# Kernel tuning notes

Measured on AMD Instinct MI355X. Metric: run time of the kernel, lower is better.

The kernel has to match this reference:

```python
import jax, jax.numpy as jnp
import numpy as np

MARGIN = 50.0

def setup_inputs() -> dict:
    key = jax.random.key(0)
    k1, k2 = jax.random.split(key)
    N, D = 4096, 768
    rep_anchor = jax.random.normal(k1, (N, D), dtype=jnp.float32)
    rep_pos = jax.random.normal(k2, (N, D), dtype=jnp.float32)
    return {"rep_anchor": rep_anchor, "rep_pos": rep_pos}

def reference(rep_anchor, rep_pos):
    # pairwise euclidean distances: dist[i, j] = ||anchor_i - pos_j||_2
    # (F.pairwise_distance with p=2, eps handled implicitly; use stable sqrt)
    a2 = jnp.sum(rep_anchor * rep_anchor, axis=1, keepdims=True)   # [N,1]
    p2 = jnp.sum(rep_pos * rep_pos, axis=1, keepdims=True).T       # [1,N]
    cross = rep_anchor @ rep_pos.T                                  # [N,N]
    sq = jnp.maximum(a2 + p2 - 2.0 * cross, 0.0)
    dist = jnp.sqrt(sq + 1e-12)
    scores = MARGIN - dist                                          # [N,N]
    # row-wise negative log-softmax, take diagonal (positive pair at index i)
    logp = jax.nn.log_softmax(scores, axis=1)
    loss_per_row = -jnp.diagonal(logp)                               # [N]
    return loss_per_row.mean()
```

## Files before the change

### kernel.cpp

```cpp
#include <hip/hip_runtime.h>
#include <hip/hip_bf16.h>
#include <hip/hip_fp8.h>
#include <stdint.h>


#define N_ROWS 4096
#define D_DIM  768
#define GRID_DIM (N_ROWS / 128)
#define NITER (D_DIM / 64)
#define BUFB  (128 * 64)

typedef float f32x4 __attribute__((ext_vector_type(4)));
typedef int   i32x4 __attribute__((ext_vector_type(4)));

__global__ __launch_bounds__(256) void cvt_norms(
        const float* __restrict__ A, const float* __restrict__ P,
        uint8_t* __restrict__ A8, uint8_t* __restrict__ P8,
        float* __restrict__ a2, float* __restrict__ p2, float* __restrict__ S) {
    const int t = threadIdx.x, lane = t & 63, wave = t >> 6;
    const int row = blockIdx.x * 4 + wave;
    const float* src = blockIdx.y ? P : A;
    uint8_t* dst = blockIdx.y ? P8 : A8;
    float* nrm = blockIdx.y ? p2 : a2;

    const float4* s4 = (const float4*)src + (size_t)row * (D_DIM / 4);
    uint32_t* d4 = (uint32_t*)dst + (size_t)row * (D_DIM / 4);
    float s = 0.0f;
#pragma unroll
    for (int c = 0; c < 3; c++) {
        const int wf = c * 64 + lane;
        float4 v = s4[wf];
        s += v.x * v.x + v.y * v.y + v.z * v.z + v.w * v.w;
        union { uint32_t u; uint8_t b[4]; } pk;
        pk.b[0] = __hip_fp8_e4m3(v.x).__x;
        pk.b[1] = __hip_fp8_e4m3(v.y).__x;
        pk.b[2] = __hip_fp8_e4m3(v.z).__x;
        pk.b[3] = __hip_fp8_e4m3(v.w).__x;
        const int kb = wf >> 4, w16 = wf & 15;
        const int gw = w16 >> 1, h = w16 & 1;
        const int gp = ((gw & 3) << 1) | (gw >> 2);
        d4[(kb << 4) + (gp << 1) + h] = pk.u;
    }
    for (int off = 32; off; off >>= 1) s += __shfl_down(s, off);
    if (lane == 0) {
        nrm[row] = s;
        if (blockIdx.y == 0) S[row] = 0.0f;
    }
}

__device__ __forceinline__ void g2l16(const void* g, void* l) {
    __builtin_amdgcn_global_load_lds(
        (const __attribute__((address_space(1))) void*)g,
        (__attribute__((address_space(3))) void*)l, 16, 0, 0);
}

__global__ __launch_bounds__(256) void gemm_fused(
        const uint8_t* __restrict__ A8, const uint8_t* __restrict__ P8,
        const float* __restrict__ a2, const float* __restrict__ p2,
        float* __restrict__ S, float* __restrict__ Dd) {
    __shared__ __align__(16) uint8_t As[3 * BUFB];
    __shared__ __align__(16) uint8_t Bs[3 * BUFB];

    const int bm = blockIdx.x, bn = blockIdx.y;
    const int t = threadIdx.x;
    const int lane = t & 63, wave = t >> 6;
    const int wm = wave >> 1, wn = wave & 1;

    f32x4 acc[4][4];
#pragma unroll
    for (int i = 0; i < 4; i++)
#pragma unroll
        for (int j = 0; j < 4; j++) acc[i][j] = (f32x4){0.f, 0.f, 0.f, 0.f};

    const int gT = ((t & 3) - (t >> 3)) & 3;
    const size_t aBase = (size_t)(bm * 128 + (t >> 2)) * D_DIM + (size_t)gT * 16;
    const size_t bBase = (size_t)(bn * 128 + (t >> 2)) * D_DIM + (size_t)gT * 16;

    const int fr = lane & 15, fq = lane >> 4;
    int aOff[4], bOff[4];
#pragma unroll
    for (int mi = 0; mi < 4; mi++) {
        const int R = wm * 64 + mi * 16 + fr;
        aOff[mi] = R * 64 + ((fq + (R >> 1)) & 3) * 16;
    }
#pragma unroll
    for (int ni = 0; ni < 4; ni++) {
        const int R = wn * 64 + ni * 16 + fr;
        bOff[ni] = R * 64 + ((fq + (R >> 1)) & 3) * 16;
    }

#define STAGE(K2, SEL)                                                            \
    do {                                                                          \
        const int k0_ = (K2) * 64;                                                \
        const int lb_ = (SEL) * BUFB;                                             \
        _Pragma("unroll")                                                         \
        for (int c = 0; c < 2; c++)                                               \
            g2l16(A8 + aBase + (size_t)c * (64 * D_DIM) + k0_,                    \
                  &As[lb_ + (c * 256 + t) * 16]);                                 \
        _Pragma("unroll")                                                         \
        for (int c = 0; c < 2; c++)                                               \
            g2l16(P8 + bBase + (size_t)c * (64 * D_DIM) + k0_,                    \
                  &Bs[lb_ + (c * 256 + t) * 16]);                                 \
    } while (0)

    STAGE(0, 0);
    STAGE(1, 1);

    int s0 = 0;
    for (int k = 0; k < NITER; k++) {
        if (k == NITER - 1) asm volatile("s_waitcnt vmcnt(0)" ::: "memory");
        else                asm volatile("s_waitcnt vmcnt(4)" ::: "memory");
        asm volatile("s_barrier" ::: "memory");
        if (k + 2 < NITER) {
            int s2 = s0 + 2; if (s2 >= 3) s2 -= 3;
            STAGE(k + 2, s2);
        }

        const int lb = s0 * BUFB;
        i32x4 av[4], bv[4];
#pragma unroll
        for (int mi = 0; mi < 4; mi++)
            av[mi] = *(const i32x4*)&As[lb + aOff[mi]];
#pragma unroll
        for (int ni = 0; ni < 4; ni++)
            bv[ni] = *(const i32x4*)&Bs[lb + bOff[ni]];
#pragma unroll
        for (int step = 0; step < 2; step++) {
#pragma unroll
            for (int mi = 0; mi < 4; mi++) {
                const long long afh = ((const long long*)&av[mi])[step];
#pragma unroll
                for (int ni = 0; ni < 4; ni++) {
                    const long long bfh = ((const long long*)&bv[ni])[step];
                    acc[mi][ni] = __builtin_amdgcn_mfma_f32_16x16x32_fp8_fp8(
                        afh, bfh, acc[mi][ni], 0, 0, 0);
                }
            }
        }
        s0 = (s0 == 2) ? 0 : s0 + 1;
    }
#undef STAGE

    float p2v[4];
#pragma unroll
    for (int ni = 0; ni < 4; ni++)
        p2v[ni] = p2[bn * 128 + wn * 64 + ni * 16 + fr];
    const int colBase = bn * 128 + wn * 64 + fr;

#pragma unroll
    for (int mi = 0; mi < 4; mi++) {
#pragma unroll
        for (int r = 0; r < 4; r++) {
            const int gi = bm * 128 + wm * 64 + mi * 16 + fq * 4 + r;
            const float a2v = a2[gi];
            float rs = 0.0f;
#pragma unroll
            for (int ni = 0; ni < 4; ni++) {
                const float cross = acc[mi][ni][r];
                const float sq = a2v + p2v[ni] - 2.0f * cross;
                const float dist = sqrtf(fmaxf(sq, 0.0f) + 1e-12f);
                const int gj = colBase + ni * 16;
                if (gi == gj) Dd[gi] = dist;
                rs += __expf(-dist);
            }
            rs += __shfl_xor(rs, 1);
            rs += __shfl_xor(rs, 2);
            rs += __shfl_xor(rs, 4);
            rs += __shfl_xor(rs, 8);
            if (fr == 0) atomicAdd(&S[gi], rs);
        }
    }
}

__global__ void finalize(const float* __restrict__ S, const float* __restrict__ Dd,
                         float* __restrict__ out) {
    const int t = threadIdx.x;
    float s = 0.0f;
    for (int i = t; i < N_ROWS; i += 256) s += Dd[i] + logf(S[i]);
    for (int off = 32; off; off >>= 1) s += __shfl_down(s, off);
    __shared__ float wsum[4];
    if ((t & 63) == 0) wsum[t >> 6] = s;
    __syncthreads();
    if (t == 0) out[0] = (wsum[0] + wsum[1] + wsum[2] + wsum[3]) * (1.0f / N_ROWS);
}

__global__ void zero_out1(float* __restrict__ out) {
    if (threadIdx.x == 0 && blockIdx.x == 0) out[0] = 0.0f;
}
__global__ void naive_row(const float* __restrict__ A, const float* __restrict__ P,
                          float* __restrict__ out) {
    __shared__ float arow[D_DIM];
    const int i = blockIdx.x, t = threadIdx.x;
    for (int c = t; c < D_DIM; c += 256) arow[c] = A[(size_t)i * D_DIM + c];
    __syncthreads();
    float sumexp = 0.0f, ddiag = 0.0f;
    for (int j = t; j < N_ROWS; j += 256) {
        const float* p = P + (size_t)j * D_DIM;
        float d2 = 0.0f;
        for (int c = 0; c < D_DIM; c++) { float df = arow[c] - p[c]; d2 += df * df; }
        float dist = sqrtf(fmaxf(d2, 0.0f) + 1e-12f);
        if (j == i) ddiag = dist;
        sumexp += __expf(-dist);
    }
    for (int off = 32; off; off >>= 1) {
        sumexp += __shfl_down(sumexp, off);
        ddiag  += __shfl_down(ddiag, off);
    }
    __shared__ float w1[4], w2[4];
    if ((t & 63) == 0) { w1[t >> 6] = sumexp; w2[t >> 6] = ddiag; }
    __syncthreads();
    if (t == 0) {
        float se = w1[0] + w1[1] + w1[2] + w1[3];
        float dd = w2[0] + w2[1] + w2[2] + w2[3];
        atomicAdd(out, (dd + logf(se)) * (1.0f / N_ROWS));
    }
}

extern "C" void kernel_launch(void* const* d_in, const int* in_sizes, int n_in,
                              void* d_out, int out_size, void* d_ws, size_t ws_size,
                              hipStream_t stream) {
    const float* A = (const float*)d_in[0];
    const float* P = (const float*)d_in[1];
    float* out = (float*)d_out;

    const size_t F8_BYTES = (size_t)N_ROWS * D_DIM;
    const size_t V_BYTES  = (size_t)N_ROWS * sizeof(float);
    const size_t NEED = 2 * F8_BYTES + 4 * V_BYTES;

    if (ws_size >= NEED) {
        char* ws = (char*)d_ws;
        uint8_t* A8 = (uint8_t*)(ws);
        uint8_t* P8 = (uint8_t*)(ws + F8_BYTES);
        float* a2 = (float*)(ws + 2 * F8_BYTES);
        float* p2 = (float*)(ws + 2 * F8_BYTES + V_BYTES);
        float* S  = (float*)(ws + 2 * F8_BYTES + 2 * V_BYTES);
        float* Dd = (float*)(ws + 2 * F8_BYTES + 3 * V_BYTES);

        hipLaunchKernelGGL(cvt_norms, dim3(N_ROWS / 4, 2), dim3(256), 0, stream,
                           A, P, A8, P8, a2, p2, S);
        hipLaunchKernelGGL(gemm_fused, dim3(GRID_DIM, GRID_DIM), dim3(256), 0, stream,
                           A8, P8, a2, p2, S, Dd);
        hipLaunchKernelGGL(finalize, dim3(1), dim3(256), 0, stream, S, Dd, out);
    } else {
        hipLaunchKernelGGL(zero_out1, dim3(1), dim3(64), 0, stream, out);
        hipLaunchKernelGGL(naive_row, dim3(N_ROWS), dim3(256), 0, stream, A, P, out);
    }
}
```

Before: 114.3 us.

## Switch to 32x32x64 scaled FP8 MFMA with XOR-swizzled LDS and tile swizzle

Replaces the 16x16x32 FP8 MFMA with the gfx950 32x32x64 f8f6f4 scaled MFMA using unit scales, quartering the MFMA instruction count per k-step. The fp8 conversion kernel now writes a plain row-major layout, and the GEMM uses an XOR-swizzled LDS layout to avoid bank conflicts for the new fragment shape. The 2D grid becomes a 1D grid with a block-index swizzle meant to improve L2 reuse. The epilogue is remapped to the 32x32 accumulator layout and adds one more shuffle stage for the row reduction.

```diff
diff --git a/kernel.cpp b/kernel.cpp
--- a/kernel.cpp
+++ b/kernel.cpp
@@ -6,12 +6,12 @@
 
 #define N_ROWS 4096
 #define D_DIM  768
-#define GRID_DIM (N_ROWS / 128)
 #define NITER (D_DIM / 64)
 #define BUFB  (128 * 64)
 
-typedef float f32x4 __attribute__((ext_vector_type(4)));
-typedef int   i32x4 __attribute__((ext_vector_type(4)));
+typedef float f32x16 __attribute__((ext_vector_type(16)));
+typedef int   i32x4  __attribute__((ext_vector_type(4)));
+typedef int   i32x8  __attribute__((ext_vector_type(8)));
 
 __global__ __launch_bounds__(256) void cvt_norms(
         const float* __restrict__ A, const float* __restrict__ P,
@@ -36,10 +36,7 @@
         pk.b[1] = __hip_fp8_e4m3(v.y).__x;
         pk.b[2] = __hip_fp8_e4m3(v.z).__x;
         pk.b[3] = __hip_fp8_e4m3(v.w).__x;
-        const int kb = wf >> 4, w16 = wf & 15;
-        const int gw = w16 >> 1, h = w16 & 1;
-        const int gp = ((gw & 3) << 1) | (gw >> 2);
-        d4[(kb << 4) + (gp << 1) + h] = pk.u;
+        d4[wf] = pk.u;
     }
     for (int off = 32; off; off >>= 1) s += __shfl_down(s, off);
     if (lane == 0) {
@@ -61,32 +58,53 @@
     __shared__ __align__(16) uint8_t As[3 * BUFB];
     __shared__ __align__(16) uint8_t Bs[3 * BUFB];
 
-    const int bm = blockIdx.x, bn = blockIdx.y;
+    const int lin = blockIdx.x;
+    const int swz = (lin & 7) * 128 + (lin >> 3);
+    const int bm = swz & 31, bn = swz >> 5;
+
     const int t = threadIdx.x;
     const int lane = t & 63, wave = t >> 6;
     const int wm = wave >> 1, wn = wave & 1;
-
-    f32x4 acc[4][4];
-#pragma unroll
-    for (int i = 0; i < 4; i++)
-#pragma unroll
-        for (int j = 0; j < 4; j++) acc[i][j] = (f32x4){0.f, 0.f, 0.f, 0.f};
-
-    const int gT = ((t & 3) - (t >> 3)) & 3;
-    const size_t aBase = (size_t)(bm * 128 + (t >> 2)) * D_DIM + (size_t)gT * 16;
-    const size_t bBase = (size_t)(bn * 128 + (t >> 2)) * D_DIM + (size_t)gT * 16;
-
-    const int fr = lane & 15, fq = lane >> 4;
-    int aOff[4], bOff[4];
-#pragma unroll
-    for (int mi = 0; mi < 4; mi++) {
-        const int R = wm * 64 + mi * 16 + fr;
-        aOff[mi] = R * 64 + ((fq + (R >> 1)) & 3) * 16;
-    }
-#pragma unroll
-    for (int ni = 0; ni < 4; ni++) {
-        const int R = wn * 64 + ni * 16 + fr;
-        bOff[ni] = R * 64 + ((fq + (R >> 1)) & 3) * 16;
+    const int r5 = lane & 31, hi = lane >> 5;
+
+    f32x16 acc[2][2];
+#pragma unroll
+    for (int i = 0; i < 2; i++)
+#pragma unroll
+        for (int j = 0; j < 2; j++)
+#pragma unroll
+            for (int r = 0; r < 16; r++) acc[i][j][r] = 0.0f;
+
+    int srcOff[2];
+#pragma unroll
+    for (int c = 0; c < 2; c++) {
+        const int q = c * 256 + t;
+        const int line = q >> 3;
+        const int slin = (q & 7) ^ (line & 7);
+        const int R = line * 2 + (slin >> 2);
+        srcOff[c] = R * D_DIM + (slin & 3) * 16;
+    }
+    const uint8_t* aG = A8 + (size_t)bm * 128 * D_DIM;
+    const uint8_t* bG = P8 + (size_t)bn * 128 * D_DIM;
+
+    int aOff[2][2], bOff[2][2];
+#pragma unroll
+    for (int mi = 0; mi < 2; mi++) {
+        const int R = wm * 64 + mi * 32 + r5;
+        const int line = R >> 1;
+        const int slb = (R & 1) * 4 + hi * 2;
+#pragma unroll
+        for (int p = 0; p < 2; p++)
+            aOff[mi][p] = line * 128 + (((slb + p) ^ (line & 7)) << 4);
+    }
+#pragma unroll
+    for (int ni = 0; ni < 2; ni++) {
+        const int R = wn * 64 + ni * 32 + r5;
+        const int line = R >> 1;
+        const int slb = (R & 1) * 4 + hi * 2;
+#pragma unroll
+        for (int p = 0; p < 2; p++)
+            bOff[ni][p] = line * 128 + (((slb + p) ^ (line & 7)) << 4);
     }
 
 #define STAGE(K2, SEL)                                                            \
@@ -95,16 +113,16 @@
         const int lb_ = (SEL) * BUFB;                                             \
         _Pragma("unroll")                                                         \
         for (int c = 0; c < 2; c++)                                               \
-            g2l16(A8 + aBase + (size_t)c * (64 * D_DIM) + k0_,                    \
-                  &As[lb_ + (c * 256 + t) * 16]);                                 \
+            g2l16(aG + srcOff[c] + k0_, &As[lb_ + (c * 256 + t) * 16]);           \
         _Pragma("unroll")                                                         \
         for (int c = 0; c < 2; c++)                                               \
-            g2l16(P8 + bBase + (size_t)c * (64 * D_DIM) + k0_,                    \
-                  &Bs[lb_ + (c * 256 + t) * 16]);                                 \
+            g2l16(bG + srcOff[c] + k0_, &Bs[lb_ + (c * 256 + t) * 16]);           \
     } while (0)
 
     STAGE(0, 0);
     STAGE(1, 1);
+
+    const int SCALE1 = 0x7f7f7f7f;
 
     int s0 = 0;
     for (int k = 0; k < NITER; k++) {
@@ -117,49 +135,51 @@
         }
 
         const int lb = s0 * BUFB;
-        i32x4 av[4], bv[4];
-#pragma unroll
-        for (int mi = 0; mi < 4; mi++)
-            av[mi] = *(const i32x4*)&As[lb + aOff[mi]];
-#pragma unroll
-        for (int ni = 0; ni < 4; ni++)
-            bv[ni] = *(const i32x4*)&Bs[lb + bOff[ni]];
-#pragma unroll
-        for (int step = 0; step < 2; step++) {
-#pragma unroll
-            for (int mi = 0; mi < 4; mi++) {
-                const long long afh = ((const long long*)&av[mi])[step];
-#pragma unroll
-                for (int ni = 0; ni < 4; ni++) {
-                    const long long bfh = ((const long long*)&bv[ni])[step];
-                    acc[mi][ni] = __builtin_amdgcn_mfma_f32_16x16x32_fp8_fp8(
-                        afh, bfh, acc[mi][ni], 0, 0, 0);
-                }
-            }
-        }
+        i32x8 af[2], bf[2];
+#pragma unroll
+        for (int mi = 0; mi < 2; mi++) {
+            const i32x4 lo = *(const i32x4*)&As[lb + aOff[mi][0]];
+            const i32x4 hi4 = *(const i32x4*)&As[lb + aOff[mi][1]];
+            af[mi][0] = lo[0]; af[mi][1] = lo[1]; af[mi][2] = lo[2]; af[mi][3] = lo[3];
+            af[mi][4] = hi4[0]; af[mi][5] = hi4[1]; af[mi][6] = hi4[2]; af[mi][7] = hi4[3];
+        }
+#pragma unroll
+        for (int ni = 0; ni < 2; ni++) {
+            const i32x4 lo = *(const i32x4*)&Bs[lb + bOff[ni][0]];
+            const i32x4 hi4 = *(const i32x4*)&Bs[lb + bOff[ni][1]];
+            bf[ni][0] = lo[0]; bf[ni][1] = lo[1]; bf[ni][2] = lo[2]; bf[ni][3] = lo[3];
+            bf[ni][4] = hi4[0]; bf[ni][5] = hi4[1]; bf[ni][6] = hi4[2]; bf[ni][7] = hi4[3];
+        }
+#pragma unroll
+        for (int mi = 0; mi < 2; mi++)
+#pragma unroll
+            for (int ni = 0; ni < 2; ni++)
+                acc[mi][ni] = __builtin_amdgcn_mfma_scale_f32_32x32x64_f8f6f4(
+                    af[mi], bf[ni], acc[mi][ni], 0, 0, 0, SCALE1, 0, SCALE1);
         s0 = (s0 == 2) ? 0 : s0 + 1;
     }
 #undef STAGE
 
-    float p2v[4];
-#pragma unroll
-    for (int ni = 0; ni < 4; ni++)
-        p2v[ni] = p2[bn * 128 + wn * 64 + ni * 16 + fr];
-    const int colBase = bn * 128 + wn * 64 + fr;
-
-#pragma unroll
-    for (int mi = 0; mi < 4; mi++) {
-#pragma unroll
-        for (int r = 0; r < 4; r++) {
-            const int gi = bm * 128 + wm * 64 + mi * 16 + fq * 4 + r;
+    float p2v[2];
+#pragma unroll
+    for (int ni = 0; ni < 2; ni++)
+        p2v[ni] = p2[bn * 128 + wn * 64 + ni * 32 + r5];
+    const int colBase = bn * 128 + wn * 64 + r5;
+
+#pragma unroll
+    for (int mi = 0; mi < 2; mi++) {
+#pragma unroll
+        for (int reg = 0; reg < 16; reg++) {
+            const int gi = bm * 128 + wm * 64 + mi * 32 +
+                           (reg & 3) + 8 * (reg >> 2) + 4 * hi;
             const float a2v = a2[gi];
             float rs = 0.0f;
 #pragma unroll
-            for (int ni = 0; ni < 4; ni++) {
-                const float cross = acc[mi][ni][r];
+            for (int ni = 0; ni < 2; ni++) {
+                const float cross = acc[mi][ni][reg];
                 const float sq = a2v + p2v[ni] - 2.0f * cross;
                 const float dist = sqrtf(fmaxf(sq, 0.0f) + 1e-12f);
-                const int gj = colBase + ni * 16;
+                const int gj = colBase + ni * 32;
                 if (gi == gj) Dd[gi] = dist;
                 rs += __expf(-dist);
             }
@@ -167,7 +187,8 @@
             rs += __shfl_xor(rs, 2);
             rs += __shfl_xor(rs, 4);
             rs += __shfl_xor(rs, 8);
-            if (fr == 0) atomicAdd(&S[gi], rs);
+            rs += __shfl_xor(rs, 16);
+            if (r5 == 0) atomicAdd(&S[gi], rs);
         }
     }
 }
@@ -238,7 +259,7 @@
 
         hipLaunchKernelGGL(cvt_norms, dim3(N_ROWS / 4, 2), dim3(256), 0, stream,
                            A, P, A8, P8, a2, p2, S);
-        hipLaunchKernelGGL(gemm_fused, dim3(GRID_DIM, GRID_DIM), dim3(256), 0, stream,
+        hipLaunchKernelGGL(gemm_fused, dim3(32 * 32), dim3(256), 0, stream,
                            A8, P8, a2, p2, S, Dd);
         hipLaunchKernelGGL(finalize, dim3(1), dim3(256), 0, stream, S, Dd, out);
     } else {
```

Measured after the change: 177.3 us. 55.1% more time.
